# Performance work log

Measured on AMD Instinct MI355X. Metric: run time of the kernel, lower is better.

## Reference

```python
import jax, jax.numpy as jnp
import numpy as np

B, S, H = 4, 8192, 1024


def setup_inputs() -> dict:
    key = jax.random.key(0)
    kq, kk, kv, k1, k2, k3, k4 = jax.random.split(key, 7)
    residual_init_factor = 1.0
    return {
        "q": jax.random.normal(kq, (B, S, H), dtype=jnp.float32),
        "k": jax.random.normal(kk, (B, S, H), dtype=jnp.float32),
        "v": jax.random.normal(kv, (B, S, H), dtype=jnp.float32),
        "w_q": 0.01 * jax.random.normal(k1, (H, H), dtype=jnp.float32),
        "w_k": 0.01 * jax.random.normal(k2, (H, H), dtype=jnp.float32),
        "w_v": 0.01 * jax.random.normal(k3, (H, H), dtype=jnp.float32),
        "w_p": 0.01 * residual_init_factor * jax.random.normal(k4, (H, H), dtype=jnp.float32),
    }


def reference(q, k, v, w_q, w_k, w_v, w_p):
    # Projections: [B,S,H] @ [H,H]
    emb_q = jnp.einsum("bsh,hd->bsd", q, w_q)
    emb_k = jnp.einsum("bsh,hd->bsd", k, w_k)
    emb_v = jnp.einsum("bsh,hd->bsd", v, w_v)
    # AFT-simple: per-channel exponential-weighted causal prefix average
    k_exp = jnp.exp(emb_k)
    k_exp_prefix = jnp.cumsum(k_exp, axis=1)
    k_exp_v_prefix = jnp.cumsum(k_exp * emb_v, axis=1)
    y = jax.nn.sigmoid(emb_q) * (k_exp_v_prefix / k_exp_prefix)
    return jnp.einsum("bsh,hd->bsd", y, w_p)
```

## Files before the change

### kernel.cpp

```cpp
#include <hip/hip_runtime.h>
#include <hip/hip_bf16.h>
#include <cstdint>

#define AS_GLOBAL __attribute__((address_space(1)))
#define AS_LDS    __attribute__((address_space(3)))

typedef __attribute__((ext_vector_type(8))) short bf16x8;
typedef __attribute__((ext_vector_type(8))) unsigned short u16x8;
typedef __attribute__((ext_vector_type(4))) float f32x4;

static __device__ __forceinline__ ushort f2bf(float x) {
    union { float f; uint32_t u; } c;
    c.f = x;
    uint32_t u = c.u;
    u += 0x7fffu + ((u >> 16) & 1u);
    return (ushort)(u >> 16);
}
static __device__ __forceinline__ float bf2f(ushort u) {
    union { uint32_t i; float f; } c;
    c.i = ((uint32_t)u) << 16;
    return c.f;
}

static __device__ __forceinline__ void gload_lds16(const void* g, void* l) {
    __builtin_amdgcn_global_load_lds(
        (const AS_GLOBAL uint32_t*)(uintptr_t)g,
        (AS_LDS uint32_t*)(uint32_t)(uintptr_t)l,
        16, 0, 0);
}

__global__ __launch_bounds__(256)
void cvt_f32_bf16(const float4* __restrict__ in, u16x8* __restrict__ out, int n8) {
    int i = blockIdx.x * 256 + threadIdx.x;
    int stride = gridDim.x * 256;
    for (; i < n8; i += stride) {
        float4 a = in[i * 2], b = in[i * 2 + 1];
        u16x8 o;
        o[0] = f2bf(a.x); o[1] = f2bf(a.y); o[2] = f2bf(a.z); o[3] = f2bf(a.w);
        o[4] = f2bf(b.x); o[5] = f2bf(b.y); o[6] = f2bf(b.z); o[7] = f2bf(b.w);
        out[i] = o;
    }
}

__global__ __launch_bounds__(256)
void transpose4_to_bf16(const float* __restrict__ w0, const float* __restrict__ w1,
                        const float* __restrict__ w2, const float* __restrict__ w3,
                        ushort* __restrict__ t0, ushort* __restrict__ t1,
                        ushort* __restrict__ t2, ushort* __restrict__ t3) {
    const int K = 1024, N = 1024;
    __shared__ float tile[32][33];
    const float* w; ushort* wt;
    switch (blockIdx.z) {
        case 0: w = w0; wt = t0; break;
        case 1: w = w1; wt = t1; break;
        case 2: w = w2; wt = t2; break;
        default: w = w3; wt = t3; break;
    }
    int bn = blockIdx.x * 32;
    int bk = blockIdx.y * 32;
    int tx = threadIdx.x & 31, ty = threadIdx.x >> 5;
    #pragma unroll
    for (int i = 0; i < 32; i += 8)
        tile[ty + i][tx] = w[(size_t)(bk + ty + i) * N + bn + tx];
    __syncthreads();
    #pragma unroll
    for (int i = 0; i < 32; i += 8)
        wt[(size_t)(bn + ty + i) * K + bk + tx] = f2bf(tile[tx][ty + i]);
}

template<int EPI, int OUT_BF>
__global__ __launch_bounds__(512, 2)
void gemm8p(const ushort* __restrict__ A, const ushort* __restrict__ Bt,
            void* __restrict__ Cv) {
    constexpr int K = 1024, N = 1024;
    __shared__ alignas(16) ushort sA[2][16384];
    __shared__ alignas(16) ushort sB[2][16384];
    const int tid  = threadIdx.x;
    const int wid  = tid >> 6;
    const int lane = tid & 63;
    const int wr = wid >> 2, wc = wid & 3;
    const int lr = lane & 15;
    const int kb = lane >> 4;
    const int x7 = lr & 7;

    const int wg = blockIdx.x;
    const int xcd = wg & 7, local = wg >> 3;
    const int bm = xcd * 16 + (local >> 2);
    const int bn = local & 3;
    const int m0 = bm * 256, n0 = bn * 256;

    f32x4 acc[8][4] = {};
    bf16x8 af[4][2];
    bf16x8 bv0[2][2], bv1[2][2];

    auto stageA = [&](int tile, int buf, int mh) {
        const int kt0 = tile * 64;
        #pragma unroll
        for (int j = 0; j < 2; j++) {
            int c = j * 512 + tid;
            int rl = c >> 3, p = c & 7;
            int s = p ^ (rl & 7);
            int gr = (rl >> 6) * 128 + mh * 64 + (rl & 63);
            gload_lds16(A + (size_t)(m0 + gr) * K + kt0 + s * 8,
                        &sA[buf][mh * 8192 + c * 8]);
        }
    };
    auto stageB = [&](int tile, int buf, int nh) {
        const int kt0 = tile * 64;
        #pragma unroll
        for (int j = 0; j < 2; j++) {
            int c = j * 512 + tid;
            int cl = c >> 3, p = c & 7;
            int s = p ^ (cl & 7);
            int gc = (cl >> 5) * 64 + nh * 32 + (cl & 31);
            gload_lds16(Bt + (size_t)(n0 + gc) * K + kt0 + s * 8,
                        &sB[buf][nh * 8192 + c * 8]);
        }
    };
    auto readA = [&](int buf, int mq) {
        #pragma unroll
        for (int m = 0; m < 4; m++)
            #pragma unroll
            for (int kh = 0; kh < 2; kh++)
                af[m][kh] = *(const bf16x8*)&sA[buf][mq * 8192
                              + (wr * 64 + m * 16 + lr) * 64
                              + ((kh * 4 + kb) ^ x7) * 8];
    };
    auto readB = [&](bf16x8 (&dst)[2][2], int buf, int nq) {
        #pragma unroll
        for (int n = 0; n < 2; n++)
            #pragma unroll
            for (int kh = 0; kh < 2; kh++)
                dst[n][kh] = *(const bf16x8*)&sB[buf][nq * 8192
                              + (wc * 32 + n * 16 + lr) * 64
                              + ((kh * 4 + kb) ^ x7) * 8];
    };
    auto mfma16 = [&](bf16x8 (&BV)[2][2], int mq, int nq) {
        #pragma unroll
        for (int m = 0; m < 4; m++)
            #pragma unroll
            for (int n = 0; n < 2; n++) {
                acc[mq*4+m][nq*2+n] = __builtin_amdgcn_mfma_f32_16x16x32_bf16(
                    af[m][0], BV[n][0], acc[mq*4+m][nq*2+n], 0, 0, 0);
                acc[mq*4+m][nq*2+n] = __builtin_amdgcn_mfma_f32_16x16x32_bf16(
                    af[m][1], BV[n][1], acc[mq*4+m][nq*2+n], 0, 0, 0);
            }
    };

#define PHASE(BV, MQ, NQ, READS, STAGES, ENDW) { \
    READS \
    STAGES \
    asm volatile("" ::: "memory"); \
    __builtin_amdgcn_s_barrier(); \
    asm volatile("s_waitcnt lgkmcnt(0)" ::: "memory"); \
    __builtin_amdgcn_s_setprio(1); \
    mfma16(BV, MQ, NQ); \
    __builtin_amdgcn_s_setprio(0); \
    ENDW \
    asm volatile("" ::: "memory"); \
    __builtin_amdgcn_s_barrier(); \
    asm volatile("" ::: "memory"); \
}

    stageA(0, 0, 0); stageA(0, 0, 1); stageB(0, 0, 0); stageB(0, 0, 1);
    stageA(1, 1, 0); stageA(1, 1, 1); stageB(1, 1, 0); stageB(1, 1, 1);
    asm volatile("s_waitcnt vmcnt(0)" ::: "memory");
    __builtin_amdgcn_s_barrier();
    asm volatile("" ::: "memory");

    for (int i = 0; i < 8; i++) {
        const int t = 2 * i;
        const int bt = t & 1, bt1 = bt ^ 1;
        PHASE(bv0, 0, 0,
            { readA(bt, 0); readB(bv0, bt, 0); },
            { if (i > 0) stageA(t + 1, bt1, 0); },
            { })
        PHASE(bv1, 0, 1,
            { readB(bv1, bt, 1); },
            { if (i > 0) stageA(t + 1, bt1, 1); },
            { asm volatile("s_waitcnt vmcnt(8)" ::: "memory"); })
        PHASE(bv0, 1, 0,
            { readA(bt, 1); },
            { if (i < 7) stageB(t + 2, bt, 0); },
            { })
        PHASE(bv1, 1, 1,
            { },
            { if (i < 7) stageB(t + 2, bt, 1); },
            { if (i < 7) asm volatile("s_waitcnt vmcnt(6)" ::: "memory");
              else       asm volatile("s_waitcnt vmcnt(0)" ::: "memory"); })
        PHASE(bv0, 0, 0,
            { readA(bt1, 0); readB(bv0, bt1, 0); },
            { if (i < 7) stageA(t + 2, bt, 0); },
            { })
        PHASE(bv1, 0, 1,
            { readB(bv1, bt1, 1); },
            { if (i < 7) stageA(t + 2, bt, 1); },
            { if (i < 7) asm volatile("s_waitcnt vmcnt(8)" ::: "memory"); })
        PHASE(bv0, 1, 0,
            { readA(bt1, 1); },
            { if (i < 7) stageB(t + 3, bt1, 0); },
            { })
        PHASE(bv1, 1, 1,
            { },
            { if (i < 7) stageB(t + 3, bt1, 1); },
            { if (i < 7) asm volatile("s_waitcnt vmcnt(6)" ::: "memory"); })
    }
#undef PHASE

    float*  Cf = (float*)Cv;
    ushort* Cb = (ushort*)Cv;
    #pragma unroll
    for (int am = 0; am < 8; am++) {
        #pragma unroll
        for (int an = 0; an < 4; an++) {
            #pragma unroll
            for (int r = 0; r < 4; r++) {
                int row = m0 + wr * 128 + (am >> 2) * 64 + (am & 3) * 16 + (lane >> 4) * 4 + r;
                int col = n0 + wc * 64 + (an >> 1) * 32 + (an & 1) * 16 + lr;
                float v = acc[am][an][r];
                if (EPI == 1) v = 1.0f / (1.0f + __expf(-v));
                else if (EPI == 2) v = __expf(v);
                size_t idx = (size_t)row * N + col;
                if (OUT_BF) Cb[idx] = f2bf(v);
                else        Cf[idx] = v;
            }
        }
    }
}

__global__ __launch_bounds__(256)
void scan_partials(const ushort* __restrict__ ke, const ushort* __restrict__ ev,
                   float* __restrict__ pke, float* __restrict__ pkv) {
    const int H = 1024, S = 8192, CHUNK = 32, BH = 4096;
    int c  = blockIdx.x * 2 + (threadIdx.x >> 7);
    int h0 = (threadIdx.x & 127) * 8;
    int b  = blockIdx.y;
    size_t base = ((size_t)b * S + (size_t)c * CHUNK) * H + h0;
    float se[8] = {}, sv[8] = {};
    for (int s = 0; s < CHUNK; s++) {
        u16x8 e8 = *(const u16x8*)(ke + base + (size_t)s * H);
        u16x8 v8 = *(const u16x8*)(ev + base + (size_t)s * H);
        #pragma unroll
        for (int i = 0; i < 8; i++) {
            float e = bf2f(e8[i]);
            se[i] += e;
            sv[i] += e * bf2f(v8[i]);
        }
    }
    size_t p = (size_t)c * BH + b * H + h0;
    *(float4*)(pke + p)     = make_float4(se[0], se[1], se[2], se[3]);
    *(float4*)(pke + p + 4) = make_float4(se[4], se[5], se[6], se[7]);
    *(float4*)(pkv + p)     = make_float4(sv[0], sv[1], sv[2], sv[3]);
    *(float4*)(pkv + p + 4) = make_float4(sv[4], sv[5], sv[6], sv[7]);
}

__global__ __launch_bounds__(256)
void scan_offsets(float* __restrict__ pke, float* __restrict__ pkv, int nch, int BH) {
    int i = blockIdx.x * blockDim.x + threadIdx.x;
    if (i >= BH) return;
    float rke = 0.f, rkv = 0.f;
    #pragma unroll 8
    for (int c = 0; c < nch; c++) {
        size_t idx = (size_t)c * BH + i;
        float a = pke[idx], b = pkv[idx];
        pke[idx] = rke; pkv[idx] = rkv;
        rke += a; rkv += b;
    }
}

__global__ __launch_bounds__(256)
void scan_final(const ushort* __restrict__ ke, const ushort* __restrict__ ev,
                const ushort* __restrict__ sq,
                const float* __restrict__ pke, const float* __restrict__ pkv,
                ushort* __restrict__ ybf) {
    const int H = 1024, S = 8192, CHUNK = 32, BH = 4096;
    int c  = blockIdx.x * 2 + (threadIdx.x >> 7);
    int h0 = (threadIdx.x & 127) * 8;
    int b  = blockIdx.y;
    size_t p = (size_t)c * BH + b * H + h0;
    float rke[8], rkv[8];
    *(float4*)(rke)     = *(const float4*)(pke + p);
    *(float4*)(rke + 4) = *(const float4*)(pke + p + 4);
    *(float4*)(rkv)     = *(const float4*)(pkv + p);
    *(float4*)(rkv + 4) = *(const float4*)(pkv + p + 4);
    size_t base = ((size_t)b * S + (size_t)c * CHUNK) * H + h0;
    for (int s = 0; s < CHUNK; s++) {
        size_t idx = base + (size_t)s * H;
        u16x8 e8 = *(const u16x8*)(ke + idx);
        u16x8 v8 = *(const u16x8*)(ev + idx);
        u16x8 q8 = *(const u16x8*)(sq + idx);
        u16x8 o;
        #pragma unroll
        for (int i = 0; i < 8; i++) {
            float e = bf2f(e8[i]);
            rke[i] += e;
            rkv[i] += e * bf2f(v8[i]);
            o[i] = f2bf(bf2f(q8[i]) * (rkv[i] / rke[i]));
        }
        *(u16x8*)(ybf + idx) = o;
    }
}

extern "C" void kernel_launch(void* const* d_in, const int* in_sizes, int n_in,
                              void* d_out, int out_size, void* d_ws, size_t ws_size,
                              hipStream_t stream) {
    const float* q   = (const float*)d_in[0];
    const float* k   = (const float*)d_in[1];
    const float* v   = (const float*)d_in[2];
    const float* w_q = (const float*)d_in[3];
    const float* w_k = (const float*)d_in[4];
    const float* w_v = (const float*)d_in[5];
    const float* w_p = (const float*)d_in[6];
    float* out = (float*)d_out;

    const int B = 4, S = 8192, H = 1024;
    const int M = B * S;
    const size_t MH = (size_t)M * H;
    const int NCH = 256;
    const int BH = B * H;

    char* ws = (char*)d_ws;
    size_t off = 0;
    auto alloc = [&](size_t bytes) -> char* {
        char* p = ws + off;
        off += (bytes + 255) & ~(size_t)255;
        return p;
    };
    ushort* abuf = (ushort*)alloc(MH * 2);
    ushort* wqt  = (ushort*)alloc((size_t)H * H * 2);
    ushort* wkt  = (ushort*)alloc((size_t)H * H * 2);
    ushort* wvt  = (ushort*)alloc((size_t)H * H * 2);
    ushort* wpt  = (ushort*)alloc((size_t)H * H * 2);
    ushort* sqb  = (ushort*)alloc(MH * 2);
    ushort* keb  = (ushort*)alloc(MH * 2);
    ushort* evb  = (ushort*)alloc(MH * 2);
    float*  pke  = (float*)alloc((size_t)NCH * BH * 4);
    float*  pkv  = (float*)alloc((size_t)NCH * BH * 4);

    const int ngg = (M / 256) * (H / 256);
    dim3 tg(H / 32, H / 32, 4);
    dim3 gs(NCH / 2, B);
    const int n8 = (int)(MH / 8);

    transpose4_to_bf16<<<tg, 256, 0, stream>>>(w_q, w_k, w_v, w_p, wqt, wkt, wvt, wpt);

    cvt_f32_bf16<<<2048, 256, 0, stream>>>((const float4*)q, (u16x8*)abuf, n8);
    gemm8p<1, 1><<<ngg, 512, 0, stream>>>(abuf, wqt, sqb);
    cvt_f32_bf16<<<2048, 256, 0, stream>>>((const float4*)k, (u16x8*)abuf, n8);
    gemm8p<2, 1><<<ngg, 512, 0, stream>>>(abuf, wkt, keb);
    cvt_f32_bf16<<<2048, 256, 0, stream>>>((const float4*)v, (u16x8*)abuf, n8);
    gemm8p<0, 1><<<ngg, 512, 0, stream>>>(abuf, wvt, evb);

    scan_partials<<<gs, 256, 0, stream>>>(keb, evb, pke, pkv);
    scan_offsets<<<BH / 256, 256, 0, stream>>>(pke, pkv, NCH, BH);
    scan_final<<<gs, 256, 0, stream>>>(keb, evb, sqb, pke, pkv, abuf);

    gemm8p<0, 0><<<ngg, 512, 0, stream>>>(abuf, wpt, out);
}
```

Measured before the change: 530.1 us.

## Use single B fragment buffer with serpentine MFMA phase order in GEMM

Result: faster. 511.3 us, median of 2 (-3.5%).

```diff
diff --git a/kernel.cpp b/kernel.cpp
--- a/kernel.cpp
+++ b/kernel.cpp
@@ -91,7 +91,7 @@
 
     f32x4 acc[8][4] = {};
     bf16x8 af[4][2];
-    bf16x8 bv0[2][2], bv1[2][2];
+    bf16x8 bv[2][2];
 
     auto stageA = [&](int tile, int buf, int mh) {
         const int kt0 = tile * 64;
@@ -126,35 +126,35 @@
                               + (wr * 64 + m * 16 + lr) * 64
                               + ((kh * 4 + kb) ^ x7) * 8];
     };
-    auto readB = [&](bf16x8 (&dst)[2][2], int buf, int nq) {
+    auto readB = [&](int buf, int nq) {
         #pragma unroll
         for (int n = 0; n < 2; n++)
             #pragma unroll
             for (int kh = 0; kh < 2; kh++)
-                dst[n][kh] = *(const bf16x8*)&sB[buf][nq * 8192
+                bv[n][kh] = *(const bf16x8*)&sB[buf][nq * 8192
                               + (wc * 32 + n * 16 + lr) * 64
                               + ((kh * 4 + kb) ^ x7) * 8];
     };
-    auto mfma16 = [&](bf16x8 (&BV)[2][2], int mq, int nq) {
+    auto mfma16 = [&](int mq, int nq) {
         #pragma unroll
         for (int m = 0; m < 4; m++)
             #pragma unroll
             for (int n = 0; n < 2; n++) {
                 acc[mq*4+m][nq*2+n] = __builtin_amdgcn_mfma_f32_16x16x32_bf16(
-                    af[m][0], BV[n][0], acc[mq*4+m][nq*2+n], 0, 0, 0);
+                    af[m][0], bv[n][0], acc[mq*4+m][nq*2+n], 0, 0, 0);
                 acc[mq*4+m][nq*2+n] = __builtin_amdgcn_mfma_f32_16x16x32_bf16(
-                    af[m][1], BV[n][1], acc[mq*4+m][nq*2+n], 0, 0, 0);
+                    af[m][1], bv[n][1], acc[mq*4+m][nq*2+n], 0, 0, 0);
             }
     };
 
-#define PHASE(BV, MQ, NQ, READS, STAGES, ENDW) { \
+#define PHASE(MQ, NQ, READS, STAGES, ENDW) { \
     READS \
     STAGES \
     asm volatile("" ::: "memory"); \
     __builtin_amdgcn_s_barrier(); \
     asm volatile("s_waitcnt lgkmcnt(0)" ::: "memory"); \
     __builtin_amdgcn_s_setprio(1); \
-    mfma16(BV, MQ, NQ); \
+    mfma16(MQ, NQ); \
     __builtin_amdgcn_s_setprio(0); \
     ENDW \
     asm volatile("" ::: "memory"); \
@@ -171,37 +171,37 @@
     for (int i = 0; i < 8; i++) {
         const int t = 2 * i;
         const int bt = t & 1, bt1 = bt ^ 1;
-        PHASE(bv0, 0, 0,
-            { readA(bt, 0); readB(bv0, bt, 0); },
+        PHASE(0, 0,
+            { readA(bt, 0); readB(bt, 0); },
             { if (i > 0) stageA(t + 1, bt1, 0); },
+            { asm volatile("s_waitcnt vmcnt(6)" ::: "memory"); })
+        PHASE(1, 0,
+            { readA(bt, 1); },
+            { if (i > 0) stageA(t + 1, bt1, 1); },
             { })
-        PHASE(bv1, 0, 1,
-            { readB(bv1, bt, 1); },
-            { if (i > 0) stageA(t + 1, bt1, 1); },
-            { asm volatile("s_waitcnt vmcnt(8)" ::: "memory"); })
-        PHASE(bv0, 1, 0,
-            { readA(bt, 1); },
+        PHASE(1, 1,
+            { readB(bt, 1); },
             { if (i < 7) stageB(t + 2, bt, 0); },
             { })
-        PHASE(bv1, 1, 1,
-            { },
+        PHASE(0, 1,
+            { readA(bt, 0); },
             { if (i < 7) stageB(t + 2, bt, 1); },
             { if (i < 7) asm volatile("s_waitcnt vmcnt(6)" ::: "memory");
               else       asm volatile("s_waitcnt vmcnt(0)" ::: "memory"); })
-        PHASE(bv0, 0, 0,
-            { readA(bt1, 0); readB(bv0, bt1, 0); },
+        PHASE(0, 0,
+            { readA(bt1, 0); readB(bt1, 0); },
             { if (i < 7) stageA(t + 2, bt, 0); },
+            { asm volatile("s_waitcnt vmcnt(6)" ::: "memory"); })
+        PHASE(1, 0,
+            { readA(bt1, 1); },
+            { if (i < 7) stageA(t + 2, bt, 1); },
             { })
-        PHASE(bv1, 0, 1,
-            { readB(bv1, bt1, 1); },
-            { if (i < 7) stageA(t + 2, bt, 1); },
-            { if (i < 7) asm volatile("s_waitcnt vmcnt(8)" ::: "memory"); })
-        PHASE(bv0, 1, 0,
-            { readA(bt1, 1); },
+        PHASE(1, 1,
+            { readB(bt1, 1); },
             { if (i < 7) stageB(t + 3, bt1, 0); },
             { })
-        PHASE(bv1, 1, 1,
-            { },
+        PHASE(0, 1,
+            { readA(bt1, 0); },
             { if (i < 7) stageB(t + 3, bt1, 1); },
             { if (i < 7) asm volatile("s_waitcnt vmcnt(6)" ::: "memory"); })
     }
```
